# Optimization experiments

Measured on AMD Instinct MI355X. Metric: run time of the kernel, lower is better.

## Reference

```python
import jax, jax.numpy as jnp
import numpy as np

DELTA = 16
L_S = 32
HID = 8      # fast SSM hidden dim
GH = 64      # slow GRU hidden
OD = 2 * HID # slow branch output dim


def setup_inputs() -> dict:
    key = jax.random.key(0)
    ks = jax.random.split(key, 9)
    B, T = 128, 65536
    x = jax.random.normal(ks[0], (B, T), dtype=jnp.float32)
    # fast branch params: f_in: Linear(1, HID, bias=False); f_out: Linear(HID, 1, bias=False)
    w_in = jax.random.normal(ks[1], (HID,), dtype=jnp.float32) * 0.3
    w_out = jax.random.normal(ks[2], (HID,), dtype=jnp.float32) * 0.3
    # slow branch GRU (input_size=1) + output linear
    w_ih = jax.random.normal(ks[3], (3 * GH,), dtype=jnp.float32) * 0.1
    w_hh = jax.random.normal(ks[4], (3 * GH, GH), dtype=jnp.float32) * 0.1
    b_ih = jax.random.normal(ks[5], (3 * GH,), dtype=jnp.float32) * 0.1
    b_hh = jax.random.normal(ks[6], (3 * GH,), dtype=jnp.float32) * 0.1
    w_sl = jax.random.normal(ks[7], (OD, GH), dtype=jnp.float32) * 0.1
    b_sl = jax.random.normal(ks[8], (OD,), dtype=jnp.float32) * 0.1
    return {"x": x, "w_in": w_in, "w_out": w_out, "w_ih": w_ih, "w_hh": w_hh,
            "b_ih": b_ih, "b_hh": b_hh, "w_sl": w_sl, "b_sl": b_sl}


def _slow_branch(frames, w_ih, w_hh, b_ih, b_hh, w_sl, b_sl):
    # frames: (B, F, L_S). GRU over the L_S samples of each frame, last hidden -> Linear.
    B, F, L = frames.shape
    seq = frames.reshape(B * F, L).T  # (L, B*F), time-major

    def gru_step(h, xt):
        gi = xt[:, None] * w_ih[None, :] + b_ih          # (N, 3GH)
        gh = h @ w_hh.T + b_hh                            # (N, 3GH)
        ir, iz, inn = jnp.split(gi, 3, axis=-1)
        hr, hz, hn = jnp.split(gh, 3, axis=-1)
        r = jax.nn.sigmoid(ir + hr)
        z = jax.nn.sigmoid(iz + hz)
        n = jnp.tanh(inn + r * hn)
        h = (1.0 - z) * n + z * h
        return h, None

    h0 = jnp.zeros((B * F, GH), dtype=frames.dtype)
    hT, _ = jax.lax.scan(gru_step, h0, seq)
    eps = hT @ w_sl.T + b_sl                              # (B*F, OD)
    return eps.reshape(B, F, OD)


def reference(x, w_in, w_out, w_ih, w_hh, b_ih, b_hh, w_sl, b_sl):
    B, T = x.shape
    F = (T - L_S) // DELTA + 1
    # x.unfold(1, 32, delta) -> gather frames (B, F, L_S)
    idx = jnp.arange(F)[:, None] * DELTA + jnp.arange(L_S)[None, :]
    frames = x[:, idx]                                    # (B, F, L_S)
    eps = _slow_branch(frames, w_ih, w_hh, b_ih, b_hh, w_sl, b_sl)
    A_s = jax.nn.sigmoid(eps[..., :HID])                  # (B, F, H)
    g_s = eps[..., HID:]                                  # (B, F, H)
    # per-timestep frame index j = clamp(i // delta - 1, 0)
    j = jnp.clip(jnp.arange(T) // DELTA - 1, 0, F - 1)
    A_t = A_s[:, j]                                       # (B, T, H)
    g_t = g_s[:, j]                                       # (B, T, H)
    # x_emb = f_in(x) * g  (f_in has no bias)
    u_t = x[:, :, None] * w_in[None, None, :] * g_t       # (B, T, H)

    def step(h, inp):
        A, u = inp
        h = A * h + u
        return h, h

    h0 = jnp.zeros((B, HID), dtype=x.dtype)
    _, hs = jax.lax.scan(step, h0, (A_t.transpose(1, 0, 2), u_t.transpose(1, 0, 2)))  # hs: (T, B, H)
    y = jnp.einsum('tbh,h->bt', hs, w_out)                # f_out, no bias
    return y
```

## Files before the change

kernel.cpp:

```cpp
#include <hip/hip_runtime.h>
#include <hip/hip_bf16.h>
#include <math.h>

#define B_SZ 128
#define T_SZ 65536
#define F_FR 4095
#define GHID 64
#define HID 8
#define CHUNK 256
#define NCH (T_SZ / CHUNK)

typedef _Float16 half8 __attribute__((ext_vector_type(8)));
typedef float f32x4 __attribute__((ext_vector_type(4)));

#define L2E 1.4426950408889634f

static __device__ __forceinline__ float frcp(float v) {
#if __has_builtin(__builtin_amdgcn_rcpf)
    return __builtin_amdgcn_rcpf(v);
#else
    return 1.0f / v;
#endif
}
static __device__ __forceinline__ float fexp2(float v) {
#if __has_builtin(__builtin_amdgcn_exp2f)
    return __builtin_amdgcn_exp2f(v);
#else
    return exp2f(v);
#endif
}
__device__ __forceinline__ float sigm(float xv) { return frcp(1.0f + fexp2(-L2E * xv)); }

#define FSTR 68
#define XSTR 33

__global__ __launch_bounds__(256, 2) void gru_mfma(
    const float* __restrict__ x, const float* __restrict__ w_ih,
    const float* __restrict__ w_hh, const float* __restrict__ b_ih,
    const float* __restrict__ b_hh, const float* __restrict__ w_sl,
    const float* __restrict__ b_sl, float* __restrict__ ag)
{
    __shared__ float lds[4][2 * 16 * FSTR + 16 * XSTR];
    const int tid  = threadIdx.x;
    const int wv   = tid >> 6;
    const int lane = tid & 63;
    const int c16  = lane & 15;
    const int g    = lane >> 4;
    float* hb0 = &lds[wv][0];
    float* hb1 = hb0 + 16 * FSTR;
    float* xs  = hb1 + 16 * FSTR;
    const int tile = ((int)blockIdx.x * 4 + wv) * 16;

    half8 wf[12][2];
#pragma unroll
    for (int n = 0; n < 12; ++n) {
        const float sc = (n < 8) ? -L2E : (2.0f * L2E);
        const int gate = 16 * n + c16;
#pragma unroll
        for (int c = 0; c < 2; ++c) {
            const float4 q0 = *(const float4*)(w_hh + gate * 64 + 32 * c + 8 * g);
            const float4 q1 = *(const float4*)(w_hh + gate * 64 + 32 * c + 8 * g + 4);
            wf[n][c][0] = (_Float16)(sc * q0.x); wf[n][c][1] = (_Float16)(sc * q0.y);
            wf[n][c][2] = (_Float16)(sc * q0.z); wf[n][c][3] = (_Float16)(sc * q0.w);
            wf[n][c][4] = (_Float16)(sc * q1.x); wf[n][c][5] = (_Float16)(sc * q1.y);
            wf[n][c][6] = (_Float16)(sc * q1.z); wf[n][c][7] = (_Float16)(sc * q1.w);
        }
    }

    float wiR[4], wiZ[4], wiN[4], bR[4], bZ[4], biN[4], bhN[4];
#pragma unroll
    for (int m = 0; m < 4; ++m) {
        const int j = c16 + 16 * m;
        wiR[m] = -L2E * w_ih[j];
        wiZ[m] = -L2E * w_ih[64 + j];
        wiN[m] = 2.0f * L2E * w_ih[128 + j];
        bR[m]  = -L2E * (b_ih[j] + b_hh[j]);
        bZ[m]  = -L2E * (b_ih[64 + j] + b_hh[64 + j]);
        biN[m] = 2.0f * L2E * b_ih[128 + j];
        bhN[m] = 2.0f * L2E * b_hh[128 + j];
    }

    {
        const int s = tile + c16;
        const int b = s / F_FR;
        const int f = s % F_FR;
        const float* xp = x + (long)b * T_SZ + f * 16;
#pragma unroll
        for (int k = 0; k < 8; ++k) xs[c16 * XSTR + g * 8 + k] = xp[g * 8 + k];
    }
#pragma unroll
    for (int m = 0; m < 4; ++m)
#pragma unroll
        for (int r = 0; r < 4; ++r) hb0[(4 * g + r) * FSTR + (c16 + 16 * m)] = 0.0f;
    __syncthreads();

    const f32x4 zz = {0.0f, 0.0f, 0.0f, 0.0f};
    float ho[4][4];
#pragma unroll
    for (int m = 0; m < 4; ++m)
#pragma unroll
        for (int r = 0; r < 4; ++r) ho[m][r] = 0.0f;

#pragma unroll 2
    for (int t = 0; t < 32; ++t) {
        float* hr_ = (t & 1) ? hb1 : hb0;
        float* hw_ = (t & 1) ? hb0 : hb1;

        half8 ah[2], al[2];
#pragma unroll
        for (int c = 0; c < 2; ++c) {
            const float* rp = hr_ + c16 * FSTR + 32 * c + 8 * g;
            const float4 u0 = *(const float4*)rp;
            const float4 u1 = *(const float4*)(rp + 4);
            const float fv[8] = {u0.x, u0.y, u0.z, u0.w, u1.x, u1.y, u1.z, u1.w};
#pragma unroll
            for (int e = 0; e < 8; ++e) {
                const _Float16 hi = (_Float16)fv[e];
                ah[c][e] = hi;
                al[c][e] = (_Float16)(fv[e] - (float)hi);
            }
        }

        f32x4 acc[12];
#pragma unroll
        for (int n = 0; n < 12; ++n) {
            f32x4 a = __builtin_amdgcn_mfma_f32_16x16x32_f16(ah[0], wf[n][0], zz, 0, 0, 0);
            a = __builtin_amdgcn_mfma_f32_16x16x32_f16(al[0], wf[n][0], a, 0, 0, 0);
            a = __builtin_amdgcn_mfma_f32_16x16x32_f16(ah[1], wf[n][1], a, 0, 0, 0);
            acc[n] = __builtin_amdgcn_mfma_f32_16x16x32_f16(al[1], wf[n][1], a, 0, 0, 0);
        }

        float xt4[4];
#pragma unroll
        for (int r = 0; r < 4; ++r) xt4[r] = xs[(4 * g + r) * XSTR + t];

#pragma unroll
        for (int m = 0; m < 4; ++m) {
            const int jm = c16 + 16 * m;
#pragma unroll
            for (int r = 0; r < 4; ++r) {
                const float uR = fmaf(xt4[r], wiR[m], bR[m]) + acc[m][r];
                const float rr = frcp(1.0f + fexp2(uR));
                const float uZ = fmaf(xt4[r], wiZ[m], bZ[m]) + acc[4 + m][r];
                const float zf = frcp(1.0f + fexp2(uZ));
                const float uN = fmaf(rr, acc[8 + m][r] + bhN[m],
                                      fmaf(xt4[r], wiN[m], biN[m]));
                const float nn = fmaf(-2.0f, frcp(1.0f + fexp2(uN)), 1.0f);
                const float hnew = fmaf(zf, ho[m][r] - nn, nn);
                ho[m][r] = hnew;
                hw_[(4 * g + r) * FSTR + jm] = hnew;
            }
        }
        __syncthreads();
    }

    half8 fh[2], fl[2];
#pragma unroll
    for (int c = 0; c < 2; ++c) {
        const float* rp = hb0 + c16 * FSTR + 32 * c + 8 * g;
        const float4 u0 = *(const float4*)rp;
        const float4 u1 = *(const float4*)(rp + 4);
        const float fv[8] = {u0.x, u0.y, u0.z, u0.w, u1.x, u1.y, u1.z, u1.w};
#pragma unroll
        for (int e = 0; e < 8; ++e) {
            const _Float16 hi = (_Float16)fv[e];
            fh[c][e] = hi;
            fl[c][e] = (_Float16)(fv[e] - (float)hi);
        }
    }
    half8 wsl[2];
#pragma unroll
    for (int c = 0; c < 2; ++c) {
        const float4 q0 = *(const float4*)(w_sl + c16 * 64 + 32 * c + 8 * g);
        const float4 q1 = *(const float4*)(w_sl + c16 * 64 + 32 * c + 8 * g + 4);
        wsl[c][0] = (_Float16)q0.x; wsl[c][1] = (_Float16)q0.y;
        wsl[c][2] = (_Float16)q0.z; wsl[c][3] = (_Float16)q0.w;
        wsl[c][4] = (_Float16)q1.x; wsl[c][5] = (_Float16)q1.y;
        wsl[c][6] = (_Float16)q1.z; wsl[c][7] = (_Float16)q1.w;
    }
    f32x4 ec = __builtin_amdgcn_mfma_f32_16x16x32_f16(fh[0], wsl[0], zz, 0, 0, 0);
    ec = __builtin_amdgcn_mfma_f32_16x16x32_f16(fl[0], wsl[0], ec, 0, 0, 0);
    ec = __builtin_amdgcn_mfma_f32_16x16x32_f16(fh[1], wsl[1], ec, 0, 0, 0);
    ec = __builtin_amdgcn_mfma_f32_16x16x32_f16(fl[1], wsl[1], ec, 0, 0, 0);
    const float bs = b_sl[c16];
#pragma unroll
    for (int r = 0; r < 4; ++r) {
        float e = ec[r] + bs;
        if (c16 < 8) e = sigm(e);
        ag[(long)(tile + 4 * g + r) * 16 + c16] = e;
    }
}

__global__ __launch_bounds__(256) void fast_chunk(
    const float* __restrict__ x, const float* __restrict__ ag,
    const float* __restrict__ w_in,
    float* __restrict__ chP, float* __restrict__ chH)
{
    const int tid = blockIdx.x * 256 + threadIdx.x;
    const int b = tid / NCH, c = tid % NCH;
    float h[HID], P[HID];
#pragma unroll
    for (int i = 0; i < HID; ++i) { h[i] = 0.0f; P[i] = 1.0f; }
    const float* xp = x + (long)b * T_SZ + c * CHUNK;

#pragma unroll 1
    for (int g = 0; g < CHUNK / 16; ++g) {
        const int t0 = c * CHUNK + g * 16;
        int fr = t0 / 16 - 1; fr = max(0, min(F_FR - 1, fr));
        const float4* agp = (const float4*)(ag + ((long)b * F_FR + fr) * 16);
        const float4 a0 = agp[0], a1 = agp[1], g0 = agp[2], g1 = agp[3];
        const float A[HID]  = {a0.x, a0.y, a0.z, a0.w, a1.x, a1.y, a1.z, a1.w};
        const float Gv[HID] = {g0.x, g0.y, g0.z, g0.w, g1.x, g1.y, g1.z, g1.w};
        float wg[HID];
#pragma unroll
        for (int i = 0; i < HID; ++i) wg[i] = w_in[i] * Gv[i];
#pragma unroll
        for (int tt = 0; tt < 16; ++tt) {
            const float xt = xp[g * 16 + tt];
#pragma unroll
            for (int i = 0; i < HID; ++i) h[i] = fmaf(A[i], h[i], xt * wg[i]);
        }
#pragma unroll
        for (int i = 0; i < HID; ++i) {
            const float a2 = A[i] * A[i]; const float a4 = a2 * a2; const float a8 = a4 * a4;
            P[i] *= a8 * a8;
        }
    }
    float* pp = chP + (long)tid * HID;
    float* hp = chH + (long)tid * HID;
#pragma unroll
    for (int i = 0; i < HID; ++i) { pp[i] = P[i]; hp[i] = h[i]; }
}

__global__ __launch_bounds__(256) void chunk_scan(
    const float* __restrict__ chP, const float* __restrict__ chH,
    float* __restrict__ st)
{
    const int tid = blockIdx.x * 256 + threadIdx.x;
    if (tid >= B_SZ * HID) return;
    const int b = tid / HID, i = tid % HID;
    float h = 0.0f;
#pragma unroll 1
    for (int c = 0; c < NCH; ++c) {
        const long idx = ((long)b * NCH + c) * HID + i;
        st[idx] = h;
        h = fmaf(chP[idx], h, chH[idx]);
    }
}

__global__ __launch_bounds__(256) void fast_apply(
    const float* __restrict__ x, const float* __restrict__ ag,
    const float* __restrict__ w_in, const float* __restrict__ w_out,
    const float* __restrict__ st, float* __restrict__ y)
{
    const int tid = blockIdx.x * 256 + threadIdx.x;
    const int b = tid / NCH, c = tid % NCH;
    float h[HID];
    const float* sp = st + (long)tid * HID;
#pragma unroll
    for (int i = 0; i < HID; ++i) h[i] = sp[i];
    float wo[HID];
#pragma unroll
    for (int i = 0; i < HID; ++i) wo[i] = w_out[i];
    const float* xp = x + (long)b * T_SZ + c * CHUNK;
    float* yp = y + (long)b * T_SZ + c * CHUNK;

#pragma unroll 1
    for (int g = 0; g < CHUNK / 16; ++g) {
        const int t0 = c * CHUNK + g * 16;
        int fr = t0 / 16 - 1; fr = max(0, min(F_FR - 1, fr));
        const float4* agp = (const float4*)(ag + ((long)b * F_FR + fr) * 16);
        const float4 a0 = agp[0], a1 = agp[1], g0 = agp[2], g1 = agp[3];
        const float A[HID]  = {a0.x, a0.y, a0.z, a0.w, a1.x, a1.y, a1.z, a1.w};
        const float Gv[HID] = {g0.x, g0.y, g0.z, g0.w, g1.x, g1.y, g1.z, g1.w};
        float wg[HID];
#pragma unroll
        for (int i = 0; i < HID; ++i) wg[i] = w_in[i] * Gv[i];
#pragma unroll
        for (int tt = 0; tt < 16; ++tt) {
            const float xt = xp[g * 16 + tt];
            float acc = 0.0f;
#pragma unroll
            for (int i = 0; i < HID; ++i) {
                h[i] = fmaf(A[i], h[i], xt * wg[i]);
                acc = fmaf(h[i], wo[i], acc);
            }
            yp[g * 16 + tt] = acc;
        }
    }
}

extern "C" void kernel_launch(void* const* d_in, const int* in_sizes, int n_in,
                              void* d_out, int out_size, void* d_ws, size_t ws_size,
                              hipStream_t stream) {
    const float* x    = (const float*)d_in[0];
    const float* w_in = (const float*)d_in[1];
    const float* w_out= (const float*)d_in[2];
    const float* w_ih = (const float*)d_in[3];
    const float* w_hh = (const float*)d_in[4];
    const float* b_ih = (const float*)d_in[5];
    const float* b_hh = (const float*)d_in[6];
    const float* w_sl = (const float*)d_in[7];
    const float* b_sl = (const float*)d_in[8];
    float* y = (float*)d_out;

    float* ag  = (float*)d_ws;
    size_t off = (size_t)B_SZ * F_FR * 16;
    float* chP = ag + off;
    float* chH = chP + (size_t)B_SZ * NCH * HID;
    float* st  = chH + (size_t)B_SZ * NCH * HID;

    const int nseq = B_SZ * F_FR;
    gru_mfma<<<nseq / 64, 256, 0, stream>>>(x, w_ih, w_hh, b_ih, b_hh, w_sl, b_sl, ag);
    fast_chunk<<<(B_SZ * NCH) / 256, 256, 0, stream>>>(x, ag, w_in, chP, chH);
    chunk_scan<<<(B_SZ * HID + 255) / 256, 256, 0, stream>>>(chP, chH, st);
    fast_apply<<<(B_SZ * NCH) / 256, 256, 0, stream>>>(x, ag, w_in, w_out, st, y);
}
```

Baseline: 1.293 ms.

## Process two 16-row tiles per wave with GRU weights staged in LDS

The GRU kernel now keeps the fp16 recurrent weights in shared memory rather than in per-lane registers. Each wave handles 32 sequences as two M tiles that share each weight fragment load. The per-step block barrier and the hidden-state double buffer are removed, because each wave only touches its own private hidden-state region. The frame load is vectorised, and occupancy is pinned with waves_per_eu. In exchange, every timestep now issues LDS reads for the weights and needs more accumulator registers for the doubled tile.

```diff
diff --git a/kernel.cpp b/kernel.cpp
--- a/kernel.cpp
+++ b/kernel.cpp
@@ -32,39 +32,40 @@
 __device__ __forceinline__ float sigm(float xv) { return frcp(1.0f + fexp2(-L2E * xv)); }
 
 #define FSTR 68
-#define XSTR 33
-
-__global__ __launch_bounds__(256, 2) void gru_mfma(
+#define XSTR 34
+
+__global__ __launch_bounds__(256) __attribute__((amdgpu_waves_per_eu(2, 2)))
+void gru_mfma(
     const float* __restrict__ x, const float* __restrict__ w_ih,
     const float* __restrict__ w_hh, const float* __restrict__ b_ih,
     const float* __restrict__ b_hh, const float* __restrict__ w_sl,
     const float* __restrict__ b_sl, float* __restrict__ ag)
 {
-    __shared__ float lds[4][2 * 16 * FSTR + 16 * XSTR];
+    __shared__ _Float16 wlds[24 * 64 * 8];
+    __shared__ float hx[4][32 * FSTR + 32 * XSTR];
     const int tid  = threadIdx.x;
     const int wv   = tid >> 6;
     const int lane = tid & 63;
     const int c16  = lane & 15;
     const int g    = lane >> 4;
-    float* hb0 = &lds[wv][0];
-    float* hb1 = hb0 + 16 * FSTR;
-    float* xs  = hb1 + 16 * FSTR;
-    const int tile = ((int)blockIdx.x * 4 + wv) * 16;
-
-    half8 wf[12][2];
-#pragma unroll
-    for (int n = 0; n < 12; ++n) {
+    float* hb = &hx[wv][0];
+    float* xs = hb + 32 * FSTR;
+    const int tile = ((int)blockIdx.x * 4 + wv) * 32;
+
+#pragma unroll
+    for (int f = 0; f < 24; f += 4) {
+        const int fi = f + wv;
+        const int n = fi >> 1, c = fi & 1;
         const float sc = (n < 8) ? -L2E : (2.0f * L2E);
-        const int gate = 16 * n + c16;
-#pragma unroll
-        for (int c = 0; c < 2; ++c) {
-            const float4 q0 = *(const float4*)(w_hh + gate * 64 + 32 * c + 8 * g);
-            const float4 q1 = *(const float4*)(w_hh + gate * 64 + 32 * c + 8 * g + 4);
-            wf[n][c][0] = (_Float16)(sc * q0.x); wf[n][c][1] = (_Float16)(sc * q0.y);
-            wf[n][c][2] = (_Float16)(sc * q0.z); wf[n][c][3] = (_Float16)(sc * q0.w);
-            wf[n][c][4] = (_Float16)(sc * q1.x); wf[n][c][5] = (_Float16)(sc * q1.y);
-            wf[n][c][6] = (_Float16)(sc * q1.z); wf[n][c][7] = (_Float16)(sc * q1.w);
-        }
+        const float* wp = w_hh + (16 * n + c16) * 64 + 32 * c + 8 * g;
+        const float4 q0 = *(const float4*)wp;
+        const float4 q1 = *(const float4*)(wp + 4);
+        half8 w8;
+        w8[0] = (_Float16)(sc * q0.x); w8[1] = (_Float16)(sc * q0.y);
+        w8[2] = (_Float16)(sc * q0.z); w8[3] = (_Float16)(sc * q0.w);
+        w8[4] = (_Float16)(sc * q1.x); w8[5] = (_Float16)(sc * q1.y);
+        w8[6] = (_Float16)(sc * q1.z); w8[7] = (_Float16)(sc * q1.w);
+        *(half8*)(wlds + (fi * 64 + lane) * 8) = w8;
     }
 
     float wiR[4], wiZ[4], wiN[4], bR[4], bZ[4], biN[4], bhN[4];
@@ -81,93 +82,89 @@
     }
 
     {
-        const int s = tile + c16;
+        const int sl = lane & 31, half = lane >> 5;
+        const int s = tile + sl;
         const int b = s / F_FR;
         const int f = s % F_FR;
-        const float* xp = x + (long)b * T_SZ + f * 16;
-#pragma unroll
-        for (int k = 0; k < 8; ++k) xs[c16 * XSTR + g * 8 + k] = xp[g * 8 + k];
-    }
-#pragma unroll
-    for (int m = 0; m < 4; ++m)
-#pragma unroll
-        for (int r = 0; r < 4; ++r) hb0[(4 * g + r) * FSTR + (c16 + 16 * m)] = 0.0f;
+        const float* xp = x + (long)b * T_SZ + f * 16 + 16 * half;
+        const float4 p0 = *(const float4*)xp;
+        const float4 p1 = *(const float4*)(xp + 4);
+        const float4 p2 = *(const float4*)(xp + 8);
+        const float4 p3 = *(const float4*)(xp + 12);
+        float* xd = xs + sl * XSTR + 16 * half;
+        *(float4*)(xd)      = p0;  *(float4*)(xd + 4)  = p1;
+        *(float4*)(xd + 8)  = p2;  *(float4*)(xd + 12) = p3;
+    }
+    for (int idx = lane; idx < 32 * FSTR; idx += 64) hb[idx] = 0.0f;
     __syncthreads();
 
     const f32x4 zz = {0.0f, 0.0f, 0.0f, 0.0f};
-    float ho[4][4];
-#pragma unroll
-    for (int m = 0; m < 4; ++m)
-#pragma unroll
-        for (int r = 0; r < 4; ++r) ho[m][r] = 0.0f;
-
-#pragma unroll 2
+    float ho[2][4][4];
+#pragma unroll
+    for (int mt = 0; mt < 2; ++mt)
+#pragma unroll
+        for (int m = 0; m < 4; ++m)
+#pragma unroll
+            for (int r = 0; r < 4; ++r) ho[mt][m][r] = 0.0f;
+
+#pragma unroll 1
     for (int t = 0; t < 32; ++t) {
-        float* hr_ = (t & 1) ? hb1 : hb0;
-        float* hw_ = (t & 1) ? hb0 : hb1;
-
-        half8 ah[2], al[2];
+        half8 ah[2][2], al[2][2];
+#pragma unroll
+        for (int mt = 0; mt < 2; ++mt)
 #pragma unroll
         for (int c = 0; c < 2; ++c) {
-            const float* rp = hr_ + c16 * FSTR + 32 * c + 8 * g;
+            const float* rp = hb + (c16 + 16 * mt) * FSTR + 32 * c + 8 * g;
             const float4 u0 = *(const float4*)rp;
             const float4 u1 = *(const float4*)(rp + 4);
             const float fv[8] = {u0.x, u0.y, u0.z, u0.w, u1.x, u1.y, u1.z, u1.w};
 #pragma unroll
             for (int e = 0; e < 8; ++e) {
                 const _Float16 hi = (_Float16)fv[e];
-                ah[c][e] = hi;
-                al[c][e] = (_Float16)(fv[e] - (float)hi);
-            }
-        }
-
-        f32x4 acc[12];
+                ah[mt][c][e] = hi;
+                al[mt][c][e] = (_Float16)(fv[e] - (float)hi);
+            }
+        }
+
+        f32x4 acc[2][12];
 #pragma unroll
         for (int n = 0; n < 12; ++n) {
-            f32x4 a = __builtin_amdgcn_mfma_f32_16x16x32_f16(ah[0], wf[n][0], zz, 0, 0, 0);
-            a = __builtin_amdgcn_mfma_f32_16x16x32_f16(al[0], wf[n][0], a, 0, 0, 0);
-            a = __builtin_amdgcn_mfma_f32_16x16x32_f16(ah[1], wf[n][1], a, 0, 0, 0);
-            acc[n] = __builtin_amdgcn_mfma_f32_16x16x32_f16(al[1], wf[n][1], a, 0, 0, 0);
-        }
-
-        float xt4[4];
-#pragma unroll
-        for (int r = 0; r < 4; ++r) xt4[r] = xs[(4 * g + r) * XSTR + t];
-
-#pragma unroll
-        for (int m = 0; m < 4; ++m) {
-            const int jm = c16 + 16 * m;
-#pragma unroll
-            for (int r = 0; r < 4; ++r) {
-                const float uR = fmaf(xt4[r], wiR[m], bR[m]) + acc[m][r];
-                const float rr = frcp(1.0f + fexp2(uR));
-                const float uZ = fmaf(xt4[r], wiZ[m], bZ[m]) + acc[4 + m][r];
-                const float zf = frcp(1.0f + fexp2(uZ));
-                const float uN = fmaf(rr, acc[8 + m][r] + bhN[m],
-                                      fmaf(xt4[r], wiN[m], biN[m]));
-                const float nn = fmaf(-2.0f, frcp(1.0f + fexp2(uN)), 1.0f);
-                const float hnew = fmaf(zf, ho[m][r] - nn, nn);
-                ho[m][r] = hnew;
-                hw_[(4 * g + r) * FSTR + jm] = hnew;
-            }
-        }
-        __syncthreads();
-    }
-
-    half8 fh[2], fl[2];
-#pragma unroll
-    for (int c = 0; c < 2; ++c) {
-        const float* rp = hb0 + c16 * FSTR + 32 * c + 8 * g;
-        const float4 u0 = *(const float4*)rp;
-        const float4 u1 = *(const float4*)(rp + 4);
-        const float fv[8] = {u0.x, u0.y, u0.z, u0.w, u1.x, u1.y, u1.z, u1.w};
-#pragma unroll
-        for (int e = 0; e < 8; ++e) {
-            const _Float16 hi = (_Float16)fv[e];
-            fh[c][e] = hi;
-            fl[c][e] = (_Float16)(fv[e] - (float)hi);
-        }
-    }
+            const half8 b0 = *(const half8*)(wlds + ((2 * n + 0) * 64 + lane) * 8);
+            const half8 b1 = *(const half8*)(wlds + ((2 * n + 1) * 64 + lane) * 8);
+#pragma unroll
+            for (int mt = 0; mt < 2; ++mt) {
+                f32x4 a = __builtin_amdgcn_mfma_f32_16x16x32_f16(ah[mt][0], b0, zz, 0, 0, 0);
+                a = __builtin_amdgcn_mfma_f32_16x16x32_f16(al[mt][0], b0, a, 0, 0, 0);
+                a = __builtin_amdgcn_mfma_f32_16x16x32_f16(ah[mt][1], b1, a, 0, 0, 0);
+                acc[mt][n] = __builtin_amdgcn_mfma_f32_16x16x32_f16(al[mt][1], b1, a, 0, 0, 0);
+            }
+        }
+
+#pragma unroll
+        for (int mt = 0; mt < 2; ++mt) {
+            float xt4[4];
+#pragma unroll
+            for (int r = 0; r < 4; ++r) xt4[r] = xs[(4 * g + r + 16 * mt) * XSTR + t];
+#pragma unroll
+            for (int m = 0; m < 4; ++m) {
+                const int jm = c16 + 16 * m;
+#pragma unroll
+                for (int r = 0; r < 4; ++r) {
+                    const float uR = fmaf(xt4[r], wiR[m], bR[m]) + acc[mt][m][r];
+                    const float rr = frcp(1.0f + fexp2(uR));
+                    const float uZ = fmaf(xt4[r], wiZ[m], bZ[m]) + acc[mt][4 + m][r];
+                    const float zf = frcp(1.0f + fexp2(uZ));
+                    const float uN = fmaf(rr, acc[mt][8 + m][r] + bhN[m],
+                                          fmaf(xt4[r], wiN[m], biN[m]));
+                    const float nn = fmaf(-2.0f, frcp(1.0f + fexp2(uN)), 1.0f);
+                    const float hnew = fmaf(zf, ho[mt][m][r] - nn, nn);
+                    ho[mt][m][r] = hnew;
+                    hb[(4 * g + r + 16 * mt) * FSTR + jm] = hnew;
+                }
+            }
+        }
+    }
+
     half8 wsl[2];
 #pragma unroll
     for (int c = 0; c < 2; ++c) {
@@ -178,16 +175,33 @@
         wsl[c][4] = (_Float16)q1.x; wsl[c][5] = (_Float16)q1.y;
         wsl[c][6] = (_Float16)q1.z; wsl[c][7] = (_Float16)q1.w;
     }
-    f32x4 ec = __builtin_amdgcn_mfma_f32_16x16x32_f16(fh[0], wsl[0], zz, 0, 0, 0);
-    ec = __builtin_amdgcn_mfma_f32_16x16x32_f16(fl[0], wsl[0], ec, 0, 0, 0);
-    ec = __builtin_amdgcn_mfma_f32_16x16x32_f16(fh[1], wsl[1], ec, 0, 0, 0);
-    ec = __builtin_amdgcn_mfma_f32_16x16x32_f16(fl[1], wsl[1], ec, 0, 0, 0);
     const float bs = b_sl[c16];
 #pragma unroll
-    for (int r = 0; r < 4; ++r) {
-        float e = ec[r] + bs;
-        if (c16 < 8) e = sigm(e);
-        ag[(long)(tile + 4 * g + r) * 16 + c16] = e;
+    for (int mt = 0; mt < 2; ++mt) {
+        half8 fh[2], fl[2];
+#pragma unroll
+        for (int c = 0; c < 2; ++c) {
+            const float* rp = hb + (c16 + 16 * mt) * FSTR + 32 * c + 8 * g;
+            const float4 u0 = *(const float4*)rp;
+            const float4 u1 = *(const float4*)(rp + 4);
+            const float fv[8] = {u0.x, u0.y, u0.z, u0.w, u1.x, u1.y, u1.z, u1.w};
+#pragma unroll
+            for (int e = 0; e < 8; ++e) {
+                const _Float16 hi = (_Float16)fv[e];
+                fh[c][e] = hi;
+                fl[c][e] = (_Float16)(fv[e] - (float)hi);
+            }
+        }
+        f32x4 ec = __builtin_amdgcn_mfma_f32_16x16x32_f16(fh[0], wsl[0], zz, 0, 0, 0);
+        ec = __builtin_amdgcn_mfma_f32_16x16x32_f16(fl[0], wsl[0], ec, 0, 0, 0);
+        ec = __builtin_amdgcn_mfma_f32_16x16x32_f16(fh[1], wsl[1], ec, 0, 0, 0);
+        ec = __builtin_amdgcn_mfma_f32_16x16x32_f16(fl[1], wsl[1], ec, 0, 0, 0);
+#pragma unroll
+        for (int r = 0; r < 4; ++r) {
+            float e = ec[r] + bs;
+            if (c16 < 8) e = sigm(e);
+            ag[(long)(tile + 16 * mt + 4 * g + r) * 16 + c16] = e;
+        }
     }
 }
 
@@ -310,8 +324,7 @@
     float* chH = chP + (size_t)B_SZ * NCH * HID;
     float* st  = chH + (size_t)B_SZ * NCH * HID;
 
-    const int nseq = B_SZ * F_FR;
-    gru_mfma<<<nseq / 64, 256, 0, stream>>>(x, w_ih, w_hh, b_ih, b_hh, w_sl, b_sl, ag);
+    gru_mfma<<<4095, 256, 0, stream>>>(x, w_ih, w_hh, b_ih, b_hh, w_sl, b_sl, ag);
     fast_chunk<<<(B_SZ * NCH) / 256, 256, 0, stream>>>(x, ag, w_in, chP, chH);
     chunk_scan<<<(B_SZ * HID + 255) / 256, 256, 0, stream>>>(chP, chH, st);
     fast_apply<<<(B_SZ * NCH) / 256, 256, 0, stream>>>(x, ag, w_in, w_out, st, y);
```

New measurement: 1.363 ms. +5.4%, slower.
